# Kernel optimization log

Measured on AMD Instinct MI355X. Metric: run time of the kernel, lower is better.

The kernel has to match this reference:

```python
import jax, jax.numpy as jnp
import numpy as np


def setup_inputs() -> dict:
    key = jax.random.key(0)
    k1, k2, k3, k4 = jax.random.split(key, 4)
    B, N, K, H, D = 2, 4096, 16, 8, 64
    q = jax.random.normal(k1, (B, N, H, D), dtype=jnp.float32)
    k_neigh = jax.random.normal(k2, (B, N, K, H, D), dtype=jnp.float32)
    v_neigh = jax.random.normal(k3, (B, N, K, H, D), dtype=jnp.float32)
    geo_f = jax.random.normal(k4, (B, N, K, H, D), dtype=jnp.float32)
    return {"q": q, "k_neigh": k_neigh, "v_neigh": v_neigh, "geo_f": geo_f}


def reference(q, k_neigh, v_neigh, geo_f):
    # q: [B,N,H,D]; k_neigh/v_neigh/geo_f: [B,N,K,H,D]
    # weight_kernal == 'cos': per-channel (non-dot-product) attention score.
    # The original's q_bucket_size chunking always collapses to a single chunk
    # (bucket is reset to N when N > bucket), and subtracting weight_max before
    # softmax is a no-op (softmax is shift-invariant), so we compute directly.
    scale = q.shape[-1] ** (-0.5)
    qe = q[:, :, None, :, :]                       # [B,N,1,H,D]
    total_weight = (qe * k_neigh + qe * geo_f) * scale  # [B,N,K,H,D]
    exp_weight = jax.nn.softmax(total_weight, axis=2)   # softmax over K neighbors
    # dropout p=0.0 -> identity
    out = jnp.sum(exp_weight * v_neigh, axis=2)    # [B,N,H,D]
    return out
```

## Files before the change

### kernel.cpp

```cpp
#include <hip/hip_runtime.h>


typedef float f4_t __attribute__((ext_vector_type(4)));

__global__ __launch_bounds__(256) void geoatt_kernel(
    const float* __restrict__ q,
    const float* __restrict__ k_neigh,
    const float* __restrict__ v_neigh,
    const float* __restrict__ geo_f,
    float* __restrict__ out,
    int total4)
{
    int tid = blockIdx.x * blockDim.x + threadIdx.x;
    if (tid >= total4) return;

    const int o    = tid << 2;
    const int bn   = o >> 9;
    const int base = (bn << 13) + (o & 511);

    const f4_t qv = *reinterpret_cast<const f4_t*>(q + o) * 0.125f;

    const f4_t* kp = reinterpret_cast<const f4_t*>(k_neigh + base);
    const f4_t* gp = reinterpret_cast<const f4_t*>(geo_f   + base);
    const f4_t* vp = reinterpret_cast<const f4_t*>(v_neigh + base);

    f4_t s   = {0.f, 0.f, 0.f, 0.f};
    f4_t acc = {0.f, 0.f, 0.f, 0.f};

#pragma unroll
    for (int k = 0; k < 16; ++k) {
        const f4_t kk = kp[k * 128];
        const f4_t gg = gp[k * 128];
        const f4_t vv = vp[k * 128];
        f4_t e;
        e.x = __expf(qv.x * (kk.x + gg.x));
        e.y = __expf(qv.y * (kk.y + gg.y));
        e.z = __expf(qv.z * (kk.z + gg.z));
        e.w = __expf(qv.w * (kk.w + gg.w));
        s   += e;
        acc += e * vv;
    }

    f4_t r;
    r.x = acc.x / s.x;
    r.y = acc.y / s.y;
    r.z = acc.z / s.z;
    r.w = acc.w / s.w;
    *reinterpret_cast<f4_t*>(out + o) = r;
}

extern "C" void kernel_launch(void* const* d_in, const int* in_sizes, int n_in,
                              void* d_out, int out_size, void* d_ws, size_t ws_size,
                              hipStream_t stream) {
    const float* q       = (const float*)d_in[0];
    const float* k_neigh = (const float*)d_in[1];
    const float* v_neigh = (const float*)d_in[2];
    const float* geo_f   = (const float*)d_in[3];
    float* out = (float*)d_out;

    const int total4 = out_size / 4;
    const int block  = 256;
    const int grid   = (total4 + block - 1) / block;

    geoatt_kernel<<<grid, block, 0, stream>>>(q, k_neigh, v_neigh, geo_f, out, total4);
}
```

Measured before the change: 660.9 us.

## Use nontemporal loads, prefetch next neighbor, and process two vectors per thread

Each thread now handles two float4 slices of a row (64 threads per row) and loads k, geo and v with nontemporal loads. The next neighbour's data is software-prefetched into registers while the current exp/accumulate runs. The grid is hardcoded to the problem size and the bounds check is removed. The aim is more loads in flight and less cache pollution for this streaming kernel, at the cost of higher register use and shape-specific launch code.

```diff
diff --git a/kernel.cpp b/kernel.cpp
--- a/kernel.cpp
+++ b/kernel.cpp
@@ -2,51 +2,79 @@
 
 
 typedef float f4_t __attribute__((ext_vector_type(4)));
+
+__device__ __forceinline__ f4_t ldnt(const float* p) {
+    return __builtin_nontemporal_load(reinterpret_cast<const f4_t*>(p));
+}
 
 __global__ __launch_bounds__(256) void geoatt_kernel(
     const float* __restrict__ q,
     const float* __restrict__ k_neigh,
     const float* __restrict__ v_neigh,
     const float* __restrict__ geo_f,
-    float* __restrict__ out,
-    int total4)
+    float* __restrict__ out)
 {
-    int tid = blockIdx.x * blockDim.x + threadIdx.x;
-    if (tid >= total4) return;
+    const int tid  = blockIdx.x * 256 + threadIdx.x;
+    const int bn   = tid >> 6;
+    const int lane = tid & 63;
 
-    const int o    = tid << 2;
-    const int bn   = o >> 9;
-    const int base = (bn << 13) + (o & 511);
+    const int in_base  = bn << 13;
+    const int out_base = bn << 9;
+    const int lo = lane << 2;
+    const int hi = lo + 256;
 
-    const f4_t qv = *reinterpret_cast<const f4_t*>(q + o) * 0.125f;
+    const f4_t ql = *reinterpret_cast<const f4_t*>(q + out_base + lo) * 0.125f;
+    const f4_t qh = *reinterpret_cast<const f4_t*>(q + out_base + hi) * 0.125f;
 
-    const f4_t* kp = reinterpret_cast<const f4_t*>(k_neigh + base);
-    const f4_t* gp = reinterpret_cast<const f4_t*>(geo_f   + base);
-    const f4_t* vp = reinterpret_cast<const f4_t*>(v_neigh + base);
+    const float* kb = k_neigh + in_base;
+    const float* gb = geo_f   + in_base;
+    const float* vb = v_neigh + in_base;
 
-    f4_t s   = {0.f, 0.f, 0.f, 0.f};
-    f4_t acc = {0.f, 0.f, 0.f, 0.f};
+    f4_t kl = ldnt(kb + lo), kh = ldnt(kb + hi);
+    f4_t gl = ldnt(gb + lo), gh = ldnt(gb + hi);
+    f4_t vl = ldnt(vb + lo), vh = ldnt(vb + hi);
+
+    f4_t sl = {0.f,0.f,0.f,0.f}, sh = {0.f,0.f,0.f,0.f};
+    f4_t al = {0.f,0.f,0.f,0.f}, ah = {0.f,0.f,0.f,0.f};
 
 #pragma unroll
     for (int k = 0; k < 16; ++k) {
-        const f4_t kk = kp[k * 128];
-        const f4_t gg = gp[k * 128];
-        const f4_t vv = vp[k * 128];
-        f4_t e;
-        e.x = __expf(qv.x * (kk.x + gg.x));
-        e.y = __expf(qv.y * (kk.y + gg.y));
-        e.z = __expf(qv.z * (kk.z + gg.z));
-        e.w = __expf(qv.w * (kk.w + gg.w));
-        s   += e;
-        acc += e * vv;
+        f4_t nkl, nkh, ngl, ngh, nvl, nvh;
+        if (k < 15) {
+            const int off = (k + 1) << 9;
+            nkl = ldnt(kb + off + lo); nkh = ldnt(kb + off + hi);
+            ngl = ldnt(gb + off + lo); ngh = ldnt(gb + off + hi);
+            nvl = ldnt(vb + off + lo); nvh = ldnt(vb + off + hi);
+        }
+
+        f4_t el, eh;
+        el.x = __expf(ql.x * (kl.x + gl.x));
+        el.y = __expf(ql.y * (kl.y + gl.y));
+        el.z = __expf(ql.z * (kl.z + gl.z));
+        el.w = __expf(ql.w * (kl.w + gl.w));
+        eh.x = __expf(qh.x * (kh.x + gh.x));
+        eh.y = __expf(qh.y * (kh.y + gh.y));
+        eh.z = __expf(qh.z * (kh.z + gh.z));
+        eh.w = __expf(qh.w * (kh.w + gh.w));
+
+        sl += el;        sh += eh;
+        al += el * vl;   ah += eh * vh;
+
+        if (k < 15) {
+            kl = nkl; kh = nkh;
+            gl = ngl; gh = ngh;
+            vl = nvl; vh = nvh;
+        }
     }
 
-    f4_t r;
-    r.x = acc.x / s.x;
-    r.y = acc.y / s.y;
-    r.z = acc.z / s.z;
-    r.w = acc.w / s.w;
-    *reinterpret_cast<f4_t*>(out + o) = r;
+    f4_t rl, rh;
+    rl.x = al.x / sl.x;  rl.y = al.y / sl.y;
+    rl.z = al.z / sl.z;  rl.w = al.w / sl.w;
+    rh.x = ah.x / sh.x;  rh.y = ah.y / sh.y;
+    rh.z = ah.z / sh.z;  rh.w = ah.w / sh.w;
+
+    *reinterpret_cast<f4_t*>(out + out_base + lo) = rl;
+    *reinterpret_cast<f4_t*>(out + out_base + hi) = rh;
 }
 
 extern "C" void kernel_launch(void* const* d_in, const int* in_sizes, int n_in,
@@ -58,9 +86,6 @@
     const float* geo_f   = (const float*)d_in[3];
     float* out = (float*)d_out;
 
-    const int total4 = out_size / 4;
-    const int block  = 256;
-    const int grid   = (total4 + block - 1) / block;
-
-    geoatt_kernel<<<grid, block, 0, stream>>>(q, k_neigh, v_neigh, geo_f, out, total4);
+    const int blocks = 2048;
+    geoatt_kernel<<<blocks, 256, 0, stream>>>(q, k_neigh, v_neigh, geo_f, out);
 }
```

Result: faster. 642.0 us (-2.9%).
